# Kernel optimization log

Hardware: AMD Instinct MI355X
Metric: run time of the kernel (lower is better)

## Reference

```python
import jax, jax.numpy as jnp
import numpy as np

NUM_HEADS = 3
WIN = 7            # window_size (square)
PAD = WIN // 2     # conv / v padding


def setup_inputs() -> dict:
    key = jax.random.key(0)
    ks = jax.random.split(key, 8)
    B, C, H, W = 8, 96, 56, 56
    hd = C // NUM_HEADS  # 32
    x = jax.random.normal(ks[0], (B, C, H, W), jnp.float32)
    # qkv 1x1 conv: weight (3C, C), bias (3C,)
    w_qkv = jax.random.normal(ks[1], (3 * C, C), jnp.float32) * (C ** -0.5)
    b_qkv = jax.random.normal(ks[2], (3 * C,), jnp.float32) * 0.01
    fan_in = 2 * hd * WIN * WIN
    w_dm = jax.random.normal(ks[3], (WIN * WIN, 2 * hd, WIN, WIN), jnp.float32) * (fan_in ** -0.5)
    b_dm = jax.random.normal(ks[4], (WIN * WIN,), jnp.float32) * 0.01
    bias_table = jax.random.normal(ks[5], (WIN * WIN, NUM_HEADS), jnp.float32) * 0.02
    # proj 1x1 conv
    w_proj = jax.random.normal(ks[6], (C, C), jnp.float32) * (C ** -0.5)
    b_proj = jax.random.normal(ks[7], (C,), jnp.float32) * 0.01
    return dict(x=x, w_qkv=w_qkv, b_qkv=b_qkv, w_dm=w_dm, b_dm=b_dm,
                bias_table=bias_table, w_proj=w_proj, b_proj=b_proj)


def reference(x, w_qkv, b_qkv, w_dm, b_dm, bias_table, w_proj, b_proj):
    B, C, H, W = x.shape
    nh = NUM_HEADS
    hd = C // nh
    scale = hd ** -0.5

    # qkv 1x1 conv -> (B, 3, nh, hd, H, W)
    qkv = jnp.einsum('oc,bchw->bohw', w_qkv, x) + b_qkv[None, :, None, None]
    qkv = qkv.reshape(B, 3, nh, hd, H, W)
    q, k, v = qkv[:, 0], qkv[:, 1], qkv[:, 2]

    qk = jnp.concatenate([(q * scale).reshape(B * nh, hd, H, W),
                          k.reshape(B * nh, hd, H, W)], axis=1)
    attn = jax.lax.conv_general_dilated(
        qk, w_dm, window_strides=(1, 1), padding=[(PAD, PAD), (PAD, PAD)],
        dimension_numbers=('NCHW', 'OIHW', 'NCHW')) + b_dm[None, :, None, None]
    attn = attn.reshape(B, nh, WIN * WIN, H, W)

    # relative position bias, broadcast over spatial dims
    attn = attn + bias_table.T.reshape(1, nh, WIN * WIN, 1, 1)
    attn = jax.nn.softmax(attn, axis=2)

    # gather sliding windows of v from a zero-padded tensor
    v_pad = jnp.pad(v, ((0, 0), (0, 0), (0, 0), (PAD, PAD), (PAD, PAD)))
    vw = jnp.stack([v_pad[..., i // WIN:i // WIN + H, i % WIN:i % WIN + W]
                    for i in range(WIN * WIN)], axis=3)

    # weighted sum over window dim, merge heads back to channels
    out = jnp.sum(vw * attn[:, :, None], axis=3).reshape(B, C, H, W)

    # output 1x1 projection (dropout p=0 -> identity)
    out = jnp.einsum('oc,bchw->bohw', w_proj, out) + b_proj[None, :, None, None]
    return out
```

## Files before the change

kernel.cpp:

```cpp
#include <hip/hip_runtime.h>
#include <hip/hip_bf16.h>
#include <stdint.h>

#define BATCH 8
#define CCH 96
#define NH 3
#define HD 32
#define HGT 56
#define WID 56
#define HW 3136
#define WIN 7
#define KK 49
#define PADR 3
#define NIMG 24
#define C2 64

typedef const float* fp32p;
typedef __attribute__((ext_vector_type(8))) short bf16x8;
typedef __attribute__((ext_vector_type(16))) float f32x16;
typedef __attribute__((ext_vector_type(2))) float f32x2;
typedef unsigned short ushort_t;

__device__ __forceinline__ float bf2f_bits(unsigned u){ return __uint_as_float(u << 16); }
__device__ __forceinline__ ushort_t f2bf_bits(float f){
  __hip_bfloat16 hb = __float2bfloat16(f);
  return *(ushort_t*)&hb;
}

__global__ __launch_bounds__(256) void prep_xt_kernel(fp32p w_dm, fp32p b_dm,
    fp32p bias_table, fp32p w_qkv, fp32p w_proj, fp32p x,
    __hip_bfloat16* __restrict__ w3, float* __restrict__ bias3,
    ushort_t* __restrict__ wq3, ushort_t* __restrict__ wp3,
    ushort_t* __restrict__ xbf){
  __shared__ float lds[128*97];
  int bx = blockIdx.x;
  if (bx < 929){
    int t = bx * 256 + threadIdx.x;
    if (t < 200704){
      int j   = t & 7;
      int l   = (t >> 3) & 63;
      int mt  = (t >> 9) & 1;
      int cb  = (t >> 10) & 1;
      int pt  = t >> 11;
      int pass = pt / KK, tap = pt % KK;
      int o  = mt*32 + (l & 31);
      int ch = pass*32 + cb*16 + (l >> 5)*8 + j;
      float v = 0.f;
      if (o < KK) v = w_dm[((size_t)(o*C2 + ch))*KK + tap];
      w3[t] = __float2bfloat16(v);
    } else if (t < 200896){
      int t2 = t - 200704;
      int h = t2 >> 6;
      int o = t2 & 63;
      bias3[t2] = (o < KK) ? (b_dm[o] + bias_table[o*NH + h]) : -1e30f;
    } else if (t < 200896 + 27648){
      int i = t - 200896;
      int j = i & 7, l = (i >> 3) & 63;
      int rest = i >> 9;
      int mt = rest % 9, k = rest / 9;
      int o = mt*32 + (l & 31);
      int c = k*16 + (l >> 5)*8 + j;
      wq3[i] = f2bf_bits(w_qkv[o*CCH + c]);
    } else if (t < 200896 + 27648 + 9216){
      int i = t - 200896 - 27648;
      int j = i & 7, l = (i >> 3) & 63;
      int rest = i >> 9;
      int mt = rest % 3, k = rest / 3;
      int o = mt*32 + (l & 31);
      int c = k*16 + (l >> 5)*8 + j;
      wp3[i] = f2bf_bits(w_proj[o*CCH + c]);
    }
  } else {
    int px0 = (bx - 929) * 128;
    int tid = threadIdx.x;
    #pragma unroll
    for (int it = 0; it < 48; ++it){
      int s = tid + it*256;
      int px = s & 127;
      int c  = s >> 7;
      int gpx = px0 + px;
      int b = gpx / HW, pp = gpx % HW;
      lds[px*97 + c] = x[((size_t)b*CCH + c)*HW + pp];
    }
    __syncthreads();
    #pragma unroll
    for (int it = 0; it < 6; ++it){
      int s = tid + it*256;
      int j  = s % 12;
      int px = s / 12;
      unsigned u[4];
      #pragma unroll
      for (int q = 0; q < 4; ++q){
        float f0 = lds[px*97 + j*8 + 2*q];
        float f1 = lds[px*97 + j*8 + 2*q + 1];
        u[q] = (unsigned)f2bf_bits(f0) | ((unsigned)f2bf_bits(f1) << 16);
      }
      uint4 w4; w4.x=u[0]; w4.y=u[1]; w4.z=u[2]; w4.w=u[3];
      *(uint4*)((char*)xbf + ((size_t)(px0+px)*96 + j*8)*2) = w4;
    }
  }
}

__global__ __launch_bounds__(64) void qkv_kernel(const ushort_t* __restrict__ xbf,
    const ushort_t* __restrict__ wq3, fp32p b_qkv,
    ushort_t* __restrict__ qplane, ushort_t* __restrict__ kplane,
    ushort_t* __restrict__ v2){
  int wid = blockIdx.x;
  int g  = wid / 784;
  int pt = wid % 784;
  int l = threadIdx.x & 63, col = l & 31, hi = l >> 5;
  int px = pt*32 + col;
  int b = px / HW, pp = px % HW;

  bf16x8 B[6];
  const char* bb = (const char*)xbf + (size_t)px*192 + hi*16;
  #pragma unroll
  for (int k = 0; k < 6; ++k) B[k] = *(const bf16x8*)(bb + k*32);

  f32x16 acc[3];
  #pragma unroll
  for (int m = 0; m < 3; ++m)
    #pragma unroll
    for (int r = 0; r < 16; ++r) acc[m][r] = 0.f;

  #pragma unroll
  for (int k = 0; k < 6; ++k){
    #pragma unroll
    for (int m = 0; m < 3; ++m){
      bf16x8 A = *(const bf16x8*)((const char*)wq3 + ((size_t)((k*9 + g*3 + m)*64 + l))*16);
      acc[m] = __builtin_amdgcn_mfma_f32_32x32x16_bf16(A, B[k], acc[m], 0, 0, 0);
    }
  }
  const float scale = 0.17677669529663687f;
  ushort_t* plane = (g == 0) ? qplane : (g == 1 ? kplane : v2);
  #pragma unroll
  for (int m = 0; m < 3; ++m){
    ushort_t* dst = plane + ((size_t)((b*NH + m)*HW + pp))*32;
    #pragma unroll
    for (int q = 0; q < 4; ++q){
      int base = 8*q + 4*hi;
      float v0 = acc[m][q*4+0] + b_qkv[g*96 + m*32 + base + 0];
      float v1 = acc[m][q*4+1] + b_qkv[g*96 + m*32 + base + 1];
      float v2f = acc[m][q*4+2] + b_qkv[g*96 + m*32 + base + 2];
      float v3 = acc[m][q*4+3] + b_qkv[g*96 + m*32 + base + 3];
      if (g == 0){ v0 *= scale; v1 *= scale; v2f *= scale; v3 *= scale; }
      uint2 pk;
      pk.x = (unsigned)f2bf_bits(v0) | ((unsigned)f2bf_bits(v1) << 16);
      pk.y = (unsigned)f2bf_bits(v2f) | ((unsigned)f2bf_bits(v3) << 16);
      *(uint2*)(&dst[base]) = pk;
    }
  }
}

#define MFMA4K(Ab, Bb) \
  { _Pragma("unroll") for (int nt = 0; nt < 2; ++nt){ \
      acc[0][nt] = __builtin_amdgcn_mfma_f32_32x32x16_bf16(Ab[0], Bb[nt], acc[0][nt], 0, 0, 0); \
      acc[1][nt] = __builtin_amdgcn_mfma_f32_32x32x16_bf16(Ab[1], Bb[nt], acc[1][nt], 0, 0, 0); \
    } }

#define LOADAK(tt, Ab) \
  { const char* An_ = Abase + (size_t)(tt)*4096; \
    Ab[0] = *(const bf16x8*)(An_); \
    Ab[1] = *(const bf16x8*)(An_ + 1024); }

#define LOADBK(tt, Bb) \
  { int ky_ = (tt) / 7, kx_ = (tt) - ky_*7; \
    _Pragma("unroll") for (int nt = 0; nt < 2; ++nt){ \
      int xp_ = nt*32 + col + kx_; if (xp_ > 61) xp_ = 61; \
      int base_ = ((row + ky_)*64 + xp_)*64; \
      int sx_ = (xp_ & 3) ^ ((xp_ >> 2) & 3); \
      Bb[nt] = *(const bf16x8*)(&smem[base_ + ((((cbw << 1) | hi) ^ sx_) << 4)]); } }

#define XWRITE(A0v, A1v) \
  { _Pragma("unroll") for (int q = 0; q < 4; ++q){ \
      float4 v4; \
      v4.x=A0v[4*q+0]; v4.y=A0v[4*q+1]; v4.z=A0v[4*q+2]; v4.w=A0v[4*q+3]; \
      *(float4*)((char*)xch + slot_o*256 + (((2*q+hi) ^ xsw)<<4)) = v4; \
      v4.x=A1v[4*q+0]; v4.y=A1v[4*q+1]; v4.z=A1v[4*q+2]; v4.w=A1v[4*q+3]; \
      *(float4*)((char*)xch + slot_o*256 + (((8+2*q+hi) ^ xsw)<<4)) = v4; } }

#define XREAD(A0v, A1v) \
  { _Pragma("unroll") for (int q = 0; q < 4; ++q){ \
      float4 v4 = *(const float4*)((char*)xch + slot_s*256 + (((2*q+hi) ^ xsw)<<4)); \
      A0v[4*q+0]+=v4.x; A0v[4*q+1]+=v4.y; A0v[4*q+2]+=v4.z; A0v[4*q+3]+=v4.w; \
      v4 = *(const float4*)((char*)xch + slot_s*256 + (((8+2*q+hi) ^ xsw)<<4)); \
      A1v[4*q+0]+=v4.x; A1v[4*q+1]+=v4.y; A1v[4*q+2]+=v4.z; A1v[4*q+3]+=v4.w; } }

__global__ __launch_bounds__(256, 3) void attn_kernel(
    const ushort_t* __restrict__ qplane, const ushort_t* __restrict__ kplane,
    const __hip_bfloat16* __restrict__ w3, const float* __restrict__ bias3,
    const ushort_t* __restrict__ v2, ushort_t* __restrict__ tmp2){
  __shared__ char smem[50176];

  int d = blockIdx.x;
  int bid = (d & 7)*84 + (d >> 3);
  int n  = bid / 28;
  int y0 = (bid % 28) * 2;
  int b = n / NH, head = n % NH;
  int tid = threadIdx.x;
  int l = tid & 63, w = tid >> 6, hi = l >> 5, col = l & 31;
  int row = w >> 1;
  int cbw = w & 1;

  f32x16 acc[2][2];
  #pragma unroll
  for (int r = 0; r < 16; ++r){
    int rowv = (r & 3) + 8*(r >> 2) + 4*hi;
    float b0 = (cbw == 0) ? bias3[head*64 + rowv] : 0.f;
    float b1 = (cbw == 0) ? bias3[head*64 + 32 + rowv] : 0.f;
    #pragma unroll
    for (int nt = 0; nt < 2; ++nt){ acc[0][nt][r] = b0; acc[1][nt][r] = b1; }
  }

  for (int pass = 0; pass < 2; ++pass){
    if (pass) __syncthreads();
    const char* src = (const char*)(pass ? kplane : qplane) + (size_t)n * HW * 64;
    #pragma unroll
    for (int it = 0; it < 8; ++it){
      int s = tid + it*256;
      int c   = s & 3;
      int xp  = (s >> 2) & 63;
      int rw  = s >> 8;
      int gy = y0 - 3 + rw;
      int gx = xp - 3;
      uint4 val = {0,0,0,0};
      if ((unsigned)gy < HGT && (unsigned)gx < WID)
        val = *(const uint4*)(src + (size_t)(gy*WID + gx)*64 + c*16);
      int sw = (c ^ (xp & 3) ^ ((xp >> 2) & 3)) << 4;
      *(uint4*)(&smem[(rw*64 + xp)*64 + sw]) = val;
    }
    __syncthreads();

    const char* Abase = (const char*)w3 + (size_t)pass*KK*4096 + cbw*2048 + l*16;
    bf16x8 A0[2], A1[2], B0[2], B1[2];
    LOADAK(0, A0); LOADBK(0, B0);
    LOADAK(1, A1); LOADBK(1, B1);
    for (int t = 0; t < 48; t += 2){
      MFMA4K(A0, B0);
      LOADAK(t+2, A0); LOADBK(t+2, B0);
      MFMA4K(A1, B1);
      int t3 = (t+3 < KK) ? (t+3) : 48;
      LOADAK(t3, A1); LOADBK(t3, B1);
    }
    MFMA4K(A0, B0);
  }

  __syncthreads();
  float* xch = (float*)smem;
  int xsw = col & 15;
  {
    int slot_o = row*64 + (1-cbw)*32 + col;
    if (cbw == 0){ XWRITE(acc[0][1], acc[1][1]); }
    else         { XWRITE(acc[0][0], acc[1][0]); }
  }
  __syncthreads();
  f32x16 a0, a1;
  {
    int slot_s = row*64 + cbw*32 + col;
    if (cbw == 0){ XREAD(acc[0][0], acc[1][0]); a0 = acc[0][0]; a1 = acc[1][0]; }
    else         { XREAD(acc[0][1], acc[1][1]); a0 = acc[0][1]; a1 = acc[1][1]; }
  }

  const char* vb = (const char*)v2 + (size_t)n * HW * 64;
  uint4 vreg[8];
  #pragma unroll
  for (int it = 0; it < 8; ++it){
    int s = tid + it*256;
    int xp  = s & 63;
    int c   = (s >> 6) & 3;
    int rw  = s >> 8;
    int gy = y0 - 3 + rw;
    int gx = xp - 3;
    uint4 val = {0,0,0,0};
    if ((unsigned)gy < HGT && (unsigned)gx < WID)
      val = *(const uint4*)(vb + (size_t)(gy*WID + gx)*64 + c*16);
    vreg[it] = val;
  }

  ushort_t* Pp = (ushort_t*)&smem[32768];
  {
    float m = -1e30f;
    #pragma unroll
    for (int r = 0; r < 16; ++r){ m = fmaxf(m, a0[r]); m = fmaxf(m, a1[r]); }
    m = fmaxf(m, __shfl_xor(m, 32));
    float s = 0.f;
    #pragma unroll
    for (int r = 0; r < 16; ++r){
      a0[r] = __expf(a0[r] - m); s += a0[r];
      a1[r] = __expf(a1[r] - m); s += a1[r];
    }
    s += __shfl_xor(s, 32);
    float inv = 1.f / s;
    int pixslot = row*64 + cbw*32 + col;
    ushort_t* Pr = Pp + pixslot*68;
    #pragma unroll
    for (int q = 0; q < 4; ++q){
      int base = 8*q + 4*hi;
      uint2 pk0;
      pk0.x = (unsigned)f2bf_bits(a0[q*4+0]*inv) | ((unsigned)f2bf_bits(a0[q*4+1]*inv) << 16);
      pk0.y = (unsigned)f2bf_bits(a0[q*4+2]*inv) | ((unsigned)f2bf_bits(a0[q*4+3]*inv) << 16);
      *(uint2*)(&Pr[base]) = pk0;
      uint2 pk1;
      pk1.x = (unsigned)f2bf_bits(a1[q*4+0]*inv) | ((unsigned)f2bf_bits(a1[q*4+1]*inv) << 16);
      pk1.y = (unsigned)f2bf_bits(a1[q*4+2]*inv) | ((unsigned)f2bf_bits(a1[q*4+3]*inv) << 16);
      *(uint2*)(&Pr[32 + base]) = pk1;
    }
  }
  __syncthreads();

  #pragma unroll
  for (int it = 0; it < 8; ++it){
    int s = tid + it*256;
    int xp  = s & 63;
    int c   = (s >> 6) & 3;
    int rw  = s >> 8;
    *(uint4*)(&smem[((c*8 + rw)*64 + xp)*16]) = vreg[it];
  }
  __syncthreads();

  int ch2 = tid >> 7;
  int slot = tid & 127;
  int pr = slot >> 6, pxx = slot & 63;
  if (pxx < WID){
    f32x2 out2[8];
    #pragma unroll
    for (int i = 0; i < 8; ++i){ out2[i].x = 0.f; out2[i].y = 0.f; }
    #pragma unroll
    for (int ky = 0; ky < WIN; ++ky){
      #pragma unroll
      for (int kx = 0; kx < WIN; ++kx){
        float pw = bf2f_bits(Pp[slot*68 + ky*7 + kx]);
        f32x2 pw2; pw2.x = pw; pw2.y = pw;
        int vrow = pr + ky, xp = pxx + kx;
        #pragma unroll
        for (int ci = 0; ci < 2; ++ci){
          int cc = ch2*2 + ci;
          uint4 vv = *(const uint4*)(&smem[((cc*8 + vrow)*64 + xp)*16]);
          unsigned ua[4] = {vv.x, vv.y, vv.z, vv.w};
          #pragma unroll
          for (int q = 0; q < 4; ++q){
            f32x2 v2f;
            v2f.x = __uint_as_float(ua[q] << 16);
            v2f.y = __uint_as_float(ua[q] & 0xffff0000u);
            out2[ci*4 + q] += pw2 * v2f;
          }
        }
      }
    }
    int pp = (y0 + pr)*WID + pxx;
    ushort_t* dst = tmp2 + ((size_t)(b*HW + pp))*96 + head*32 + ch2*16;
    #pragma unroll
    for (int j2 = 0; j2 < 2; ++j2){
      unsigned u[4];
      #pragma unroll
      for (int q = 0; q < 4; ++q){
        u[q] = (unsigned)f2bf_bits(out2[j2*4 + q].x) | ((unsigned)f2bf_bits(out2[j2*4 + q].y) << 16);
      }
      uint4 w4; w4.x=u[0]; w4.y=u[1]; w4.z=u[2]; w4.w=u[3];
      *(uint4*)(&dst[j2*8]) = w4;
    }
  }
}

__global__ __launch_bounds__(64) void proj_kernel(const ushort_t* __restrict__ tmp2,
    const ushort_t* __restrict__ wp3, fp32p b_proj, float* __restrict__ outp){
  int pt = blockIdx.x;
  int l = threadIdx.x & 63, col = l & 31, hi = l >> 5;
  int px = pt*32 + col;
  int b = px / HW, pp = px % HW;

  bf16x8 B[6];
  const char* bb = (const char*)tmp2 + (size_t)px*192 + hi*16;
  #pragma unroll
  for (int k = 0; k < 6; ++k) B[k] = *(const bf16x8*)(bb + k*32);

  f32x16 acc[3];
  #pragma unroll
  for (int m = 0; m < 3; ++m)
    #pragma unroll
    for (int r = 0; r < 16; ++r) acc[m][r] = 0.f;

  #pragma unroll
  for (int k = 0; k < 6; ++k){
    #pragma unroll
    for (int m = 0; m < 3; ++m){
      bf16x8 A = *(const bf16x8*)((const char*)wp3 + ((size_t)((k*3 + m)*64 + l))*16);
      acc[m] = __builtin_amdgcn_mfma_f32_32x32x16_bf16(A, B[k], acc[m], 0, 0, 0);
    }
  }
  #pragma unroll
  for (int m = 0; m < 3; ++m){
    #pragma unroll
    for (int r = 0; r < 16; ++r){
      int o = m*32 + (r & 3) + 8*(r >> 2) + 4*hi;
      outp[((size_t)(b*CCH + o))*HW + pp] = acc[m][r] + b_proj[o];
    }
  }
}

extern "C" void kernel_launch(void* const* d_in, const int* in_sizes, int n_in,
                              void* d_out, int out_size, void* d_ws, size_t ws_size,
                              hipStream_t stream){
  fp32p x          = (fp32p)d_in[0];
  fp32p w_qkv      = (fp32p)d_in[1];
  fp32p b_qkv      = (fp32p)d_in[2];
  fp32p w_dm       = (fp32p)d_in[3];
  fp32p b_dm       = (fp32p)d_in[4];
  fp32p bias_table = (fp32p)d_in[5];
  fp32p w_proj     = (fp32p)d_in[6];
  fp32p b_proj     = (fp32p)d_in[7];

  char* ws = (char*)d_ws;
  const size_t XBF_BYTES   = (size_t)BATCH * HW * 96 * 2;
  const size_t PLANE_BYTES = (size_t)NIMG * HW * 32 * 2;
  const size_t TMP2_BYTES  = (size_t)BATCH * HW * 96 * 2;
  const size_t W3_BYTES    = 200704ull * 2;
  size_t off = 0;
  ushort_t* xbf    = (ushort_t*)(ws + off); off += XBF_BYTES;
  ushort_t* qplane = (ushort_t*)(ws + off); off += PLANE_BYTES;
  ushort_t* kplane = (ushort_t*)(ws + off); off += PLANE_BYTES;
  ushort_t* v2     = (ushort_t*)(ws + off); off += PLANE_BYTES;
  ushort_t* tmp2   = (ushort_t*)(ws + off); off += TMP2_BYTES;
  __hip_bfloat16* w3 = (__hip_bfloat16*)(ws + off); off += W3_BYTES;
  float* bias3     = (float*)(ws + off);    off += 192*4;
  ushort_t* wq3    = (ushort_t*)(ws + off); off += 27648*2;
  ushort_t* wp3    = (ushort_t*)(ws + off); off += 9216*2;

  hipLaunchKernelGGL(prep_xt_kernel, dim3(1125), dim3(256), 0, stream,
                     w_dm, b_dm, bias_table, w_qkv, w_proj, x,
                     w3, bias3, wq3, wp3, xbf);
  hipLaunchKernelGGL(qkv_kernel, dim3(2352), dim3(64), 0, stream,
                     xbf, wq3, b_qkv, qplane, kplane, v2);
  hipLaunchKernelGGL(attn_kernel, dim3(672), dim3(256), 0, stream,
                     qplane, kplane, w3, bias3, v2, tmp2);
  hipLaunchKernelGGL(proj_kernel, dim3(784), dim3(64), 0, stream,
                     tmp2, wp3, b_proj, (float*)d_out);
}
```

Baseline: 74.47 us.

## Deepen attn MFMA prefetch, vectorize P reads, merge qkv groups per block

The qkv kernel now runs the three output groups as three wavefronts of one 192-thread block instead of separate 64-thread blocks, so the same x tile is shared within a block. The attention-score MFMA loop keeps four A fragments in flight, adds compiler scheduling fences, and pads the P row stride to 72 so each pixel's 49 softmax weights can be loaded with seven 16-byte LDS reads into registers. An empty asm statement pins the prefetched V registers. These changes aim to hide global and LDS latency and cut scalar LDS loads, at the cost of higher register pressure that may hurt occupancy.

```diff
diff --git a/kernel.cpp b/kernel.cpp
--- a/kernel.cpp
+++ b/kernel.cpp
@@ -101,13 +101,12 @@
   }
 }
 
-__global__ __launch_bounds__(64) void qkv_kernel(const ushort_t* __restrict__ xbf,
+__global__ __launch_bounds__(192) void qkv_kernel(const ushort_t* __restrict__ xbf,
     const ushort_t* __restrict__ wq3, fp32p b_qkv,
     ushort_t* __restrict__ qplane, ushort_t* __restrict__ kplane,
     ushort_t* __restrict__ v2){
-  int wid = blockIdx.x;
-  int g  = wid / 784;
-  int pt = wid % 784;
+  int pt = blockIdx.x;
+  int g  = threadIdx.x >> 6;
   int l = threadIdx.x & 63, col = l & 31, hi = l >> 5;
   int px = pt*32 + col;
   int b = px / HW, pp = px % HW;
@@ -171,6 +170,8 @@
       int sx_ = (xp_ & 3) ^ ((xp_ >> 2) & 3); \
       Bb[nt] = *(const bf16x8*)(&smem[base_ + ((((cbw << 1) | hi) ^ sx_) << 4)]); } }
 
+#define SCHED_FENCE() asm volatile("" ::: "memory")
+
 #define XWRITE(A0v, A1v) \
   { _Pragma("unroll") for (int q = 0; q < 4; ++q){ \
       float4 v4; \
@@ -190,7 +191,7 @@
     const ushort_t* __restrict__ qplane, const ushort_t* __restrict__ kplane,
     const __hip_bfloat16* __restrict__ w3, const float* __restrict__ bias3,
     const ushort_t* __restrict__ v2, ushort_t* __restrict__ tmp2){
-  __shared__ char smem[50176];
+  __shared__ char smem[51200];
 
   int d = blockIdx.x;
   int bid = (d & 7)*84 + (d >> 3);
@@ -232,15 +233,25 @@
     __syncthreads();
 
     const char* Abase = (const char*)w3 + (size_t)pass*KK*4096 + cbw*2048 + l*16;
-    bf16x8 A0[2], A1[2], B0[2], B1[2];
-    LOADAK(0, A0); LOADBK(0, B0);
-    LOADAK(1, A1); LOADBK(1, B1);
-    for (int t = 0; t < 48; t += 2){
-      MFMA4K(A0, B0);
-      LOADAK(t+2, A0); LOADBK(t+2, B0);
-      MFMA4K(A1, B1);
-      int t3 = (t+3 < KK) ? (t+3) : 48;
-      LOADAK(t3, A1); LOADBK(t3, B1);
+    bf16x8 A0[2], A1[2], A2[2], A3[2], B0[2], B1[2];
+    LOADAK(0, A0); LOADAK(1, A1); LOADAK(2, A2); LOADAK(3, A3);
+    LOADBK(0, B0); LOADBK(1, B1);
+    SCHED_FENCE();
+    for (int t = 0; t < 48; t += 4){
+      int ta0 = (t+4 < KK) ? t+4 : 48;
+      int ta1 = (t+5 < KK) ? t+5 : 48;
+      int ta2 = (t+6 < KK) ? t+6 : 48;
+      int ta3 = (t+7 < KK) ? t+7 : 48;
+      int tb2 = (t+2 < KK) ? t+2 : 48;
+      int tb3 = (t+3 < KK) ? t+3 : 48;
+      int tb4 = (t+4 < KK) ? t+4 : 48;
+      int tb5 = (t+5 < KK) ? t+5 : 48;
+      MFMA4K(A0, B0); LOADBK(tb2, B0); LOADAK(ta0, A0);
+      MFMA4K(A1, B1); LOADBK(tb3, B1); LOADAK(ta1, A1);
+      SCHED_FENCE();
+      MFMA4K(A2, B0); LOADBK(tb4, B0); LOADAK(ta2, A2);
+      MFMA4K(A3, B1); LOADBK(tb5, B1); LOADAK(ta3, A3);
+      SCHED_FENCE();
     }
     MFMA4K(A0, B0);
   }
@@ -292,7 +303,7 @@
     s += __shfl_xor(s, 32);
     float inv = 1.f / s;
     int pixslot = row*64 + cbw*32 + col;
-    ushort_t* Pr = Pp + pixslot*68;
+    ushort_t* Pr = Pp + pixslot*72;
     #pragma unroll
     for (int q = 0; q < 4; ++q){
       int base = 8*q + 4*hi;
@@ -306,6 +317,9 @@
       *(uint2*)(&Pr[32 + base]) = pk1;
     }
   }
+  asm volatile("" :: "v"(vreg[0].x), "v"(vreg[1].x), "v"(vreg[2].x),
+                     "v"(vreg[3].x), "v"(vreg[4].x), "v"(vreg[5].x),
+                     "v"(vreg[6].x), "v"(vreg[7].x));
   __syncthreads();
 
   #pragma unroll
@@ -322,6 +336,12 @@
   int slot = tid & 127;
   int pr = slot >> 6, pxx = slot & 63;
   if (pxx < WID){
+    unsigned pw_[28];
+    #pragma unroll
+    for (int i = 0; i < 7; ++i){
+      uint4 v4 = *(const uint4*)(&Pp[slot*72 + i*8]);
+      pw_[i*4+0] = v4.x; pw_[i*4+1] = v4.y; pw_[i*4+2] = v4.z; pw_[i*4+3] = v4.w;
+    }
     f32x2 out2[8];
     #pragma unroll
     for (int i = 0; i < 8; ++i){ out2[i].x = 0.f; out2[i].y = 0.f; }
@@ -329,7 +349,10 @@
     for (int ky = 0; ky < WIN; ++ky){
       #pragma unroll
       for (int kx = 0; kx < WIN; ++kx){
-        float pw = bf2f_bits(Pp[slot*68 + ky*7 + kx]);
+        const int o = ky*7 + kx;
+        unsigned wv = pw_[o >> 1];
+        float pw = (o & 1) ? __uint_as_float(wv & 0xffff0000u)
+                           : __uint_as_float(wv << 16);
         f32x2 pw2; pw2.x = pw; pw2.y = pw;
         int vrow = pr + ky, xp = pxx + kx;
         #pragma unroll
@@ -429,7 +452,7 @@
   hipLaunchKernelGGL(prep_xt_kernel, dim3(1125), dim3(256), 0, stream,
                      w_dm, b_dm, bias_table, w_qkv, w_proj, x,
                      w3, bias3, wq3, wp3, xbf);
-  hipLaunchKernelGGL(qkv_kernel, dim3(2352), dim3(64), 0, stream,
+  hipLaunchKernelGGL(qkv_kernel, dim3(784), dim3(192), 0, stream,
                      xbf, wq3, b_qkv, qplane, kplane, v2);
   hipLaunchKernelGGL(attn_kernel, dim3(672), dim3(256), 0, stream,
                      qplane, kplane, w3, bias3, v2, tmp2);
```

Measured after the change: 75.12 us. No clear change (+0.9%).
